# Performance work log

Measured on AMD Instinct MI355X. Metric: run time of the kernel, lower is better.

## Reference

```python
import jax, jax.numpy as jnp
import numpy as np

B, T, C, H = 2, 2048, 1024, 16
HD = C // H  # 64


def setup_inputs() -> dict:
    key = jax.random.key(0)
    ks = jax.random.split(key, 5)
    x = jax.random.normal(ks[0], (B, T, C), jnp.float32)
    scale = 0.02
    Wq = jax.random.normal(ks[1], (C, C), jnp.float32) * scale
    Wk = jax.random.normal(ks[2], (C, C), jnp.float32) * scale
    Wv = jax.random.normal(ks[3], (C, C), jnp.float32) * scale
    Wo = jax.random.normal(ks[4], (C, C), jnp.float32) * scale
    # RoPE tables: freqs_cis = exp(i * pos * theta_j), theta_j = 10000^(-2j/HD)
    pos = jnp.arange(T, dtype=jnp.float32)
    theta = 10000.0 ** (-jnp.arange(0, HD, 2, dtype=jnp.float32) / HD)  # [HD/2]
    ang = pos[:, None] * theta[None, :]  # [T, HD/2]
    cos = jnp.cos(ang)
    sin = jnp.sin(ang)
    return {"x": x, "Wq": Wq, "Wk": Wk, "Wv": Wv, "Wo": Wo, "cos": cos, "sin": sin}


def _rope(t, cos, sin):
    # t: [B,T,H,HD]; pairs (even, odd) along last dim form complex numbers
    b, s, h, hd = t.shape
    tr = t.reshape(b, s, h, hd // 2, 2)
    t0, t1 = tr[..., 0], tr[..., 1]
    c = cos[None, :, None, :]  # [1,T,1,HD/2]
    sn = sin[None, :, None, :]
    o0 = t0 * c - t1 * sn
    o1 = t0 * sn + t1 * c
    return jnp.stack([o0, o1], axis=-1).reshape(b, s, h, hd)


def reference(x, Wq, Wk, Wv, Wo, cos, sin):
    b, t, c = x.shape
    h, hd = H, c // H
    q = (x @ Wq.T).reshape(b, t, h, hd)
    k = (x @ Wk.T).reshape(b, t, h, hd)
    v = (x @ Wv.T).reshape(b, t, h, hd)
    q = _rope(q, cos, sin)
    k = _rope(k, cos, sin)
    # explicit causal attention with full TxT score matrix (as in source)
    att = jnp.einsum("bthd,bshd->bhts", q, k) / jnp.sqrt(jnp.float32(hd))
    causal = jnp.tril(jnp.ones((t, t), dtype=bool))
    att = jnp.where(causal[None, None, :, :], att, -jnp.inf)
    att = jax.nn.softmax(att, axis=-1)
    out = jnp.einsum("bhts,bshd->bthd", att, v).reshape(b, t, c)
    return out @ Wo.T
```

## Files before the change

kernel.cpp:

```cpp
#include <hip/hip_runtime.h>
#include <cstdint>
#include <cstddef>


typedef __bf16 bf16;
typedef float  f32x4  __attribute__((ext_vector_type(4)));
typedef __bf16 bf16x4 __attribute__((ext_vector_type(4)));
typedef __bf16 bf16x8 __attribute__((ext_vector_type(8)));

constexpr int Bb = 2, Tt = 2048, Cc = 1024, Hh = 16;
constexpr int Mrows = Bb * Tt;
constexpr int NT = Tt / 64;
constexpr int LDS_ = 72;

#define GLOAD_LDS16(gp, lp)                                                      \
    __builtin_amdgcn_global_load_lds(                                            \
        (const __attribute__((address_space(1))) void*)(gp),                     \
        (__attribute__((address_space(3))) void*)(lp), 16, 0, 0)

#define QUAD_T(v0, v1, v2, v3, c2)                                               \
    {                                                                            \
        float e0 = (c2 & 1) ? v0 : v1, e1 = (c2 & 1) ? v2 : v3;                  \
        e0 = __shfl_xor(e0, 1); e1 = __shfl_xor(e1, 1);                          \
        if (c2 & 1) { v0 = e0; v2 = e1; } else { v1 = e0; v3 = e1; }             \
        float f0 = (c2 & 2) ? v0 : v2, f1 = (c2 & 2) ? v1 : v3;                  \
        f0 = __shfl_xor(f0, 2); f1 = __shfl_xor(f1, 2);                          \
        if (c2 & 2) { v0 = f0; v1 = f1; } else { v2 = f0; v3 = f1; }             \
    }

__global__ __launch_bounds__(256) void convert_k(const float* __restrict__ x,
                                                 const float* __restrict__ Wq,
                                                 const float* __restrict__ Wk,
                                                 const float* __restrict__ Wv,
                                                 const float* __restrict__ Wo,
                                                 const float* __restrict__ cosb,
                                                 const float* __restrict__ sinb,
                                                 bf16* __restrict__ xb,
                                                 bf16* __restrict__ Wqkv,
                                                 bf16* __restrict__ Wob,
                                                 float2* __restrict__ cs)
{
    if (blockIdx.x >= 4096) {
        int pi = ((blockIdx.x - 4096) * 256 + threadIdx.x) * 8;
#pragma unroll
        for (int u = 0; u < 8; ++u)
            cs[pi + u] = float2{cosb[pi + u], sinb[pi + u]};
        return;
    }
    uint32_t id = blockIdx.x * 256 + threadIdx.x;
    const float* src; bf16* dst; float sc = 1.0f;
    if (id < 524288u) {
        uint32_t tile = id >> 10, slot = id & 1023;
        uint32_t row = (tile >> 4) * 128 + (slot >> 9) * 64 +
                       ((slot >> 6) & 3) * 16 + (slot & 15);
        uint32_t k = (tile & 15) * 64 + ((slot >> 8) & 1) * 32 + ((slot >> 4) & 3) * 8;
        src = x + (size_t)row * 1024 + k;
        dst = xb + (size_t)id * 8;
    } else if (id < 917504u) {
        uint32_t t2 = id - 524288u;
        uint32_t tile = t2 >> 10, slot = t2 & 1023;
        uint32_t n = (tile >> 4) * 128 + (slot >> 9) * 64 +
                     ((slot >> 6) & 3) * 16 + (slot & 15);
        uint32_t k = (tile & 15) * 64 + ((slot >> 8) & 1) * 32 + ((slot >> 4) & 3) * 8;
        if (n < 1024)      { src = Wq + (size_t)n * 1024 + k;
                             sc = 0.125f * 1.44269504088896f; }
        else if (n < 2048)   src = Wk + (size_t)(n - 1024) * 1024 + k;
        else                 src = Wv + (size_t)(n - 2048) * 1024 + k;
        dst = Wqkv + (size_t)t2 * 8;
    } else {
        uint32_t t3 = id - 917504u;
        uint32_t tile = t3 >> 9, slot = t3 & 511;
        uint32_t n = (tile >> 4) * 64 + (slot >> 8) * 32 +
                     ((slot >> 6) & 1) * 16 + (slot & 15);
        uint32_t k = (tile & 15) * 64 + ((slot >> 7) & 1) * 32 + ((slot >> 4) & 3) * 8;
        src = Wo + (size_t)n * 1024 + k;
        dst = Wob + (size_t)t3 * 8;
    }
    float4 v0 = *(const float4*)(src);
    float4 v1 = *(const float4*)(src + 4);
    bf16x8 t;
    t[0] = (bf16)(v0.x*sc); t[1] = (bf16)(v0.y*sc); t[2] = (bf16)(v0.z*sc); t[3] = (bf16)(v0.w*sc);
    t[4] = (bf16)(v1.x*sc); t[5] = (bf16)(v1.y*sc); t[6] = (bf16)(v1.z*sc); t[7] = (bf16)(v1.w*sc);
    *(bf16x8*)dst = t;
}

__global__ __launch_bounds__(256) void gemm_qkv(const bf16* __restrict__ A,
                                                const bf16* __restrict__ W,
                                                bf16* __restrict__ QK,
                                                bf16* __restrict__ Vt,
                                                const float2* __restrict__ cs)
{
    __shared__ bf16 As[8192];
    __shared__ bf16 Ws[8192];
    const int tid  = threadIdx.x;
    const int lane = tid & 63, wave = tid >> 6;
    const int rhw = wave >> 1, chw = wave & 1;
    const int wr = rhw * 64, wc = chw * 64;
    const int l16 = lane & 15, lq = lane >> 4;
    const int row0 = blockIdx.x * 128, col0 = blockIdx.y * 128;

    f32x4 acc[4][4];
#pragma unroll
    for (int i = 0; i < 4; ++i)
#pragma unroll
        for (int j = 0; j < 4; ++j) acc[i][j] = f32x4{0.f, 0.f, 0.f, 0.f};

    const bf16* At = A + (size_t)blockIdx.x * 16 * 8192;
    const bf16* Wt = W + (size_t)blockIdx.y * 16 * 8192;

    for (int kb = 0; kb < 16; ++kb) {
        const bf16* at = At + kb * 8192;
        const bf16* wt = Wt + kb * 8192;
#pragma unroll
        for (int rnd = 0; rnd < 4; ++rnd) {
            const int seg = rnd * 4 + wave;
            GLOAD_LDS16(at + seg * 512 + lane * 8, &As[seg * 512]);
            GLOAD_LDS16(wt + seg * 512 + lane * 8, &Ws[seg * 512]);
        }
        __syncthreads();
#pragma unroll
        for (int ks = 0; ks < 2; ++ks) {
            bf16x8 af[4], bfr[4];
#pragma unroll
            for (int i = 0; i < 4; ++i)
                af[i] = *(const bf16x8*)(&As[(rhw * 512 + ks * 256 + i * 64 + lq * 16 + l16) * 8]);
#pragma unroll
            for (int j = 0; j < 4; ++j)
                bfr[j] = *(const bf16x8*)(&Ws[(chw * 512 + ks * 256 + j * 64 + lq * 16 + l16) * 8]);
#pragma unroll
            for (int i = 0; i < 4; ++i)
#pragma unroll
                for (int j = 0; j < 4; ++j)
                    acc[i][j] = __builtin_amdgcn_mfma_f32_16x16x32_bf16(
                        af[i], bfr[j], acc[i][j], 0, 0, 0);
        }
        __syncthreads();
    }

    const int c2 = l16 & 3, g4 = (l16 >> 2) * 4;
    if (blockIdx.y < 16) {
#pragma unroll
        for (int i = 0; i < 4; ++i)
#pragma unroll
            for (int j = 0; j < 4; ++j) {
                float v0 = acc[i][j][0], v1 = acc[i][j][1];
                float v2 = acc[i][j][2], v3 = acc[i][j][3];
                QUAD_T(v0, v1, v2, v3, c2);
                const int row = row0 + wr + i * 16 + lq * 4 + c2;
                const int t   = row & (Tt - 1);
                const int colb = wc + j * 16 + g4;
                const int p0   = (colb & 63) >> 1;
                float4 cp = *(const float4*)(&cs[t * 32 + p0]);
                bf16x4 pk;
                pk[0] = (bf16)(v0 * cp.x - v1 * cp.y);
                pk[1] = (bf16)(v0 * cp.y + v1 * cp.x);
                pk[2] = (bf16)(v2 * cp.z - v3 * cp.w);
                pk[3] = (bf16)(v2 * cp.w + v3 * cp.z);
                *(bf16x4*)(&QK[(size_t)row * 2048 + col0 + colb]) = pk;
            }
    } else {
#pragma unroll
        for (int i = 0; i < 4; ++i)
#pragma unroll
            for (int j = 0; j < 4; ++j) {
                const int dfull = col0 - 2048 + wc + j * 16 + l16;
                const int h = dfull >> 6, d = dfull & 63;
                const int row = row0 + wr + i * 16 + lq * 4;
                const int b = row >> 11, t = row & (Tt - 1);
                bf16x4 pk;
                pk[0] = (bf16)acc[i][j][0]; pk[1] = (bf16)acc[i][j][1];
                pk[2] = (bf16)acc[i][j][2]; pk[3] = (bf16)acc[i][j][3];
                *(bf16x4*)(&Vt[((size_t)(b * 16 + h) * 64 + d) * (size_t)Tt + t]) = pk;
            }
    }
}

__global__ __launch_bounds__(256) void gemm_o(const bf16* __restrict__ A,
                                              const bf16* __restrict__ W,
                                              float* __restrict__ Out)
{
    __shared__ bf16 As[8192];
    __shared__ bf16 Ws[4096];
    const int tid  = threadIdx.x;
    const int lane = tid & 63, wave = tid >> 6;
    const int rhw = wave >> 1, chw = wave & 1;
    const int wr = rhw * 64, wc = chw * 32;
    const int l16 = lane & 15, lq = lane >> 4;
    const int row0 = blockIdx.x * 128, col0 = blockIdx.y * 64;

    f32x4 acc[4][2];
#pragma unroll
    for (int i = 0; i < 4; ++i)
#pragma unroll
        for (int j = 0; j < 2; ++j) acc[i][j] = f32x4{0.f, 0.f, 0.f, 0.f};

    const bf16* At = A + (size_t)blockIdx.x * 16 * 8192;
    const bf16* Wt = W + (size_t)blockIdx.y * 16 * 4096;

    for (int kb = 0; kb < 16; ++kb) {
        const bf16* at = At + kb * 8192;
        const bf16* wt = Wt + kb * 4096;
#pragma unroll
        for (int rnd = 0; rnd < 4; ++rnd) {
            const int seg = rnd * 4 + wave;
            GLOAD_LDS16(at + seg * 512 + lane * 8, &As[seg * 512]);
        }
#pragma unroll
        for (int rnd = 0; rnd < 2; ++rnd) {
            const int seg = rnd * 4 + wave;
            GLOAD_LDS16(wt + seg * 512 + lane * 8, &Ws[seg * 512]);
        }
        __syncthreads();
#pragma unroll
        for (int ks = 0; ks < 2; ++ks) {
            bf16x8 af[4], bfr[2];
#pragma unroll
            for (int i = 0; i < 4; ++i)
                af[i] = *(const bf16x8*)(&As[(rhw * 512 + ks * 256 + i * 64 + lq * 16 + l16) * 8]);
#pragma unroll
            for (int j = 0; j < 2; ++j)
                bfr[j] = *(const bf16x8*)(&Ws[(chw * 256 + ks * 128 + j * 64 + lq * 16 + l16) * 8]);
#pragma unroll
            for (int i = 0; i < 4; ++i)
#pragma unroll
                for (int j = 0; j < 2; ++j)
                    acc[i][j] = __builtin_amdgcn_mfma_f32_16x16x32_bf16(
                        af[i], bfr[j], acc[i][j], 0, 0, 0);
        }
        __syncthreads();
    }
    const int c2 = l16 & 3, g4 = (l16 >> 2) * 4;
#pragma unroll
    for (int i = 0; i < 4; ++i)
#pragma unroll
        for (int j = 0; j < 2; ++j) {
            float v0 = acc[i][j][0], v1 = acc[i][j][1];
            float v2 = acc[i][j][2], v3 = acc[i][j][3];
            QUAD_T(v0, v1, v2, v3, c2);
            const int row = row0 + wr + i * 16 + lq * 4 + c2;
            const int col = col0 + wc + j * 16 + g4;
            *(float4*)(&Out[(size_t)row * Cc + col]) = float4{v0, v1, v2, v3};
        }
}

__global__ __launch_bounds__(256, 4) void attn_k(const bf16* __restrict__ QK,
                                                 const bf16* __restrict__ Vt,
                                                 bf16* __restrict__ O)
{
    __shared__ bf16 Ks[2][64 * LDS_];
    __shared__ bf16 Vs[2][64 * LDS_];
    const int tid = threadIdx.x;
    const int wv = tid >> 6, lane = tid & 63;
    const int l16 = lane & 15, lq = lane >> 4;
    const int id = blockIdx.y * 16 + blockIdx.x;
    const int bh = (id & 7) * 4 + (id >> 7);
    const int pi = (id >> 3) & 15;
    const int b = bh >> 4, h = bh & 15;
    const int kr = tid >> 2, c0 = (tid & 3) * 16;
    const int pr = 32 * (kr >> 5) + 16 * ((kr >> 2) & 1) + 4 * ((kr >> 3) & 3) + (kr & 3);

    const bf16* kcol = QK + 1024 + (size_t)(b * Tt + kr) * 2048 + h * 64 + c0;
    const bf16* vcol = Vt + ((size_t)bh * 64 + kr) * Tt + c0;

    for (int phase = 0; phase < 2; ++phase) {
        const int qt = phase ? pi : (NT - 1 - pi);

        const int qglob = qt * 64 + wv * 16 + l16;
        const bf16* qp = QK + (size_t)(b * Tt + qglob) * 2048 + h * 64;
        bf16x8 qf0 = *(const bf16x8*)(qp + lq * 8);
        bf16x8 qf1 = *(const bf16x8*)(qp + 32 + lq * 8);

        uint4 pk0 = *(const uint4*)(kcol);
        uint4 pk1 = *(const uint4*)(kcol + 8);
        uint4 pv0 = *(const uint4*)(vcol);
        uint4 pv1 = *(const uint4*)(vcol + 8);
        *(uint4*)(&Ks[0][pr * LDS_ + c0])     = pk0;
        *(uint4*)(&Ks[0][pr * LDS_ + c0 + 8]) = pk1;
        *(uint4*)(&Vs[0][kr * LDS_ + c0])     = pv0;
        *(uint4*)(&Vs[0][kr * LDS_ + c0 + 8]) = pv1;
        __syncthreads();

        float l = 0.f;
        f32x4 o[4];
#pragma unroll
        for (int dt = 0; dt < 4; ++dt) o[dt] = f32x4{0.f, 0.f, 0.f, 0.f};

        for (int t = 0; t <= qt; ++t) {
            const int cur = t & 1;
            if (t < qt) {
                const bf16* kn = kcol + (size_t)(t + 1) * 64 * 2048;
                const bf16* vn = vcol + (t + 1) * 64;
                pk0 = *(const uint4*)(kn);
                pk1 = *(const uint4*)(kn + 8);
                pv0 = *(const uint4*)(vn);
                pv1 = *(const uint4*)(vn + 8);
            }

            f32x4 s[4];
#pragma unroll
            for (int mt = 0; mt < 4; ++mt) s[mt] = f32x4{0.f, 0.f, 0.f, 0.f};
#pragma unroll
            for (int mt = 0; mt < 4; ++mt) {
                bf16x8 a0 = *(const bf16x8*)(&Ks[cur][(mt * 16 + l16) * LDS_ + lq * 8]);
                s[mt] = __builtin_amdgcn_mfma_f32_16x16x32_bf16(a0, qf0, s[mt], 0, 0, 0);
            }
#pragma unroll
            for (int mt = 0; mt < 4; ++mt) {
                bf16x8 a1 = *(const bf16x8*)(&Ks[cur][(mt * 16 + l16) * LDS_ + 32 + lq * 8]);
                s[mt] = __builtin_amdgcn_mfma_f32_16x16x32_bf16(a1, qf1, s[mt], 0, 0, 0);
            }
            if (t == qt) {
                const int qloc = wv * 16 + l16;
#pragma unroll
                for (int mt = 0; mt < 4; ++mt)
#pragma unroll
                    for (int r = 0; r < 4; ++r) {
                        int keyl = (mt >> 1) * 32 + lq * 8 + (mt & 1) * 4 + r;
                        if (keyl > qloc) s[mt][r] = -1e30f;
                    }
            }
            bf16x8 pb0, pb1;
#pragma unroll
            for (int mt = 0; mt < 4; ++mt)
#pragma unroll
                for (int r = 0; r < 4; ++r) {
                    float p = exp2f(s[mt][r]);
                    l += p;
                    s[mt][r] = p;
                }
#pragma unroll
            for (int r = 0; r < 4; ++r) {
                pb0[r]     = (bf16)s[0][r];
                pb0[4 + r] = (bf16)s[1][r];
                pb1[r]     = (bf16)s[2][r];
                pb1[4 + r] = (bf16)s[3][r];
            }
#pragma unroll
            for (int dt = 0; dt < 4; ++dt) {
                bf16x8 v0 = *(const bf16x8*)(&Vs[cur][(dt * 16 + l16) * LDS_ + lq * 8]);
                o[dt] = __builtin_amdgcn_mfma_f32_16x16x32_bf16(v0, pb0, o[dt], 0, 0, 0);
            }
#pragma unroll
            for (int dt = 0; dt < 4; ++dt) {
                bf16x8 v1 = *(const bf16x8*)(&Vs[cur][(dt * 16 + l16) * LDS_ + 32 + lq * 8]);
                o[dt] = __builtin_amdgcn_mfma_f32_16x16x32_bf16(v1, pb1, o[dt], 0, 0, 0);
            }
            if (t < qt) {
                *(uint4*)(&Ks[cur ^ 1][pr * LDS_ + c0])     = pk0;
                *(uint4*)(&Ks[cur ^ 1][pr * LDS_ + c0 + 8]) = pk1;
                *(uint4*)(&Vs[cur ^ 1][kr * LDS_ + c0])     = pv0;
                *(uint4*)(&Vs[cur ^ 1][kr * LDS_ + c0 + 8]) = pv1;
            }
            __syncthreads();
        }
        l += __shfl_xor(l, 16);
        l += __shfl_xor(l, 32);
        float inv = 1.f / l;
        bf16* obase = O + ((size_t)(b * 16 + (qt >> 1)) * 16 + h) * 8192;
        const int rh = qt & 1;
#pragma unroll
        for (int dt = 0; dt < 4; ++dt) {
            bf16x4 pk;
#pragma unroll
            for (int r = 0; r < 4; ++r) pk[r] = (bf16)(o[dt][r] * inv);
            const int slot = rh * 512 + (dt >> 1) * 256 + wv * 64 +
                             ((dt & 1) * 2 + (lq >> 1)) * 16 + l16;
            *(bf16x4*)(obase + slot * 8 + (lq & 1) * 4) = pk;
        }
    }
}

extern "C" void kernel_launch(void* const* d_in, const int* in_sizes, int n_in,
                              void* d_out, int out_size, void* d_ws, size_t ws_size,
                              hipStream_t stream)
{
    const float* x    = (const float*)d_in[0];
    const float* Wq   = (const float*)d_in[1];
    const float* Wk   = (const float*)d_in[2];
    const float* Wv   = (const float*)d_in[3];
    const float* Wo   = (const float*)d_in[4];
    const float* cosb = (const float*)d_in[5];
    const float* sinb = (const float*)d_in[6];

    constexpr size_t M1 = 1024 * 1024;
    bf16* base = (bf16*)d_ws;
    bf16*   xb   = base;
    bf16*   QK   = base + 4 * M1;
    bf16*   VtG  = base + 12 * M1;
    bf16*   Wqkv = base + 16 * M1;
    bf16*   Wob  = base + 19 * M1;
    float2* csT  = (float2*)(base + 20 * M1);
    bf16*   Ow   = xb;

    convert_k<<<4096 + 32, 256, 0, stream>>>(x, Wq, Wk, Wv, Wo, cosb, sinb,
                                             xb, Wqkv, Wob, csT);

    gemm_qkv<<<dim3(Mrows / 128, 3072 / 128), 256, 0, stream>>>(
        xb, Wqkv, QK, VtG, csT);

    attn_k<<<dim3(NT / 2, Bb * Hh), 256, 0, stream>>>(QK, VtG, Ow);

    gemm_o<<<dim3(Mrows / 128, Cc / 64), 256, 0, stream>>>(Ow, Wob, (float*)d_out);
}
```

Measured before the change: 175.5 us.

## Launch one attention block per query tile and compute row sums via MFMA

The attention kernel no longer pairs a long and a short query tile in one block. It launches one block per query tile (1024 blocks instead of 512) with a remapped id that orders tiles from heavy to light in rounds, to improve load balance and occupancy. The softmax denominator is now accumulated with an extra MFMA against a ones vector instead of scalar adds followed by cross-lane shuffles. The trade-off is two extra MFMAs per iteration and more blocks that each reload their own K/V tiles.

Result: faster. 169.2 us (-3.6%).

```diff
diff --git a/kernel.cpp b/kernel.cpp
--- a/kernel.cpp
+++ b/kernel.cpp
@@ -252,9 +252,11 @@
     const int tid = threadIdx.x;
     const int wv = tid >> 6, lane = tid & 63;
     const int l16 = lane & 15, lq = lane >> 4;
-    const int id = blockIdx.y * 16 + blockIdx.x;
-    const int bh = (id & 7) * 4 + (id >> 7);
-    const int pi = (id >> 3) & 15;
+    const int id = blockIdx.y * gridDim.x + blockIdx.x;
+    const int bh = (id & 7) * 4 + ((id >> 3) & 3);
+    const int sIdx = (id >> 5) & 7, rnd4 = id >> 8;
+    const int qt = (rnd4 == 0) ? 31 - sIdx : (rnd4 == 1) ? 16 + sIdx
+                 : (rnd4 == 2) ? 15 - sIdx : sIdx;
     const int b = bh >> 4, h = bh & 15;
     const int kr = tid >> 2, c0 = (tid & 3) * 16;
     const int pr = 32 * (kr >> 5) + 16 * ((kr >> 2) & 1) + 4 * ((kr >> 3) & 3) + (kr & 3);
@@ -262,111 +264,108 @@
     const bf16* kcol = QK + 1024 + (size_t)(b * Tt + kr) * 2048 + h * 64 + c0;
     const bf16* vcol = Vt + ((size_t)bh * 64 + kr) * Tt + c0;
 
-    for (int phase = 0; phase < 2; ++phase) {
-        const int qt = phase ? pi : (NT - 1 - pi);
-
-        const int qglob = qt * 64 + wv * 16 + l16;
-        const bf16* qp = QK + (size_t)(b * Tt + qglob) * 2048 + h * 64;
-        bf16x8 qf0 = *(const bf16x8*)(qp + lq * 8);
-        bf16x8 qf1 = *(const bf16x8*)(qp + 32 + lq * 8);
-
-        uint4 pk0 = *(const uint4*)(kcol);
-        uint4 pk1 = *(const uint4*)(kcol + 8);
-        uint4 pv0 = *(const uint4*)(vcol);
-        uint4 pv1 = *(const uint4*)(vcol + 8);
-        *(uint4*)(&Ks[0][pr * LDS_ + c0])     = pk0;
-        *(uint4*)(&Ks[0][pr * LDS_ + c0 + 8]) = pk1;
-        *(uint4*)(&Vs[0][kr * LDS_ + c0])     = pv0;
-        *(uint4*)(&Vs[0][kr * LDS_ + c0 + 8]) = pv1;
+    const int qglob = qt * 64 + wv * 16 + l16;
+    const bf16* qp = QK + (size_t)(b * Tt + qglob) * 2048 + h * 64;
+    bf16x8 qf0 = *(const bf16x8*)(qp + lq * 8);
+    bf16x8 qf1 = *(const bf16x8*)(qp + 32 + lq * 8);
+
+    bf16x8 onef;
+#pragma unroll
+    for (int r = 0; r < 8; ++r) onef[r] = (bf16)1.0f;
+
+    uint4 pk0 = *(const uint4*)(kcol);
+    uint4 pk1 = *(const uint4*)(kcol + 8);
+    uint4 pv0 = *(const uint4*)(vcol);
+    uint4 pv1 = *(const uint4*)(vcol + 8);
+    *(uint4*)(&Ks[0][pr * LDS_ + c0])     = pk0;
+    *(uint4*)(&Ks[0][pr * LDS_ + c0 + 8]) = pk1;
+    *(uint4*)(&Vs[0][kr * LDS_ + c0])     = pv0;
+    *(uint4*)(&Vs[0][kr * LDS_ + c0 + 8]) = pv1;
+    __syncthreads();
+
+    f32x4 accl = f32x4{0.f, 0.f, 0.f, 0.f};
+    f32x4 o[4];
+#pragma unroll
+    for (int dt = 0; dt < 4; ++dt) o[dt] = f32x4{0.f, 0.f, 0.f, 0.f};
+
+    for (int t = 0; t <= qt; ++t) {
+        const int cur = t & 1;
+        if (t < qt) {
+            const bf16* kn = kcol + (size_t)(t + 1) * 64 * 2048;
+            const bf16* vn = vcol + (t + 1) * 64;
+            pk0 = *(const uint4*)(kn);
+            pk1 = *(const uint4*)(kn + 8);
+            pv0 = *(const uint4*)(vn);
+            pv1 = *(const uint4*)(vn + 8);
+        }
+
+        f32x4 s[4];
+#pragma unroll
+        for (int mt = 0; mt < 4; ++mt) s[mt] = f32x4{0.f, 0.f, 0.f, 0.f};
+#pragma unroll
+        for (int mt = 0; mt < 4; ++mt) {
+            bf16x8 a0 = *(const bf16x8*)(&Ks[cur][(mt * 16 + l16) * LDS_ + lq * 8]);
+            s[mt] = __builtin_amdgcn_mfma_f32_16x16x32_bf16(a0, qf0, s[mt], 0, 0, 0);
+        }
+#pragma unroll
+        for (int mt = 0; mt < 4; ++mt) {
+            bf16x8 a1 = *(const bf16x8*)(&Ks[cur][(mt * 16 + l16) * LDS_ + 32 + lq * 8]);
+            s[mt] = __builtin_amdgcn_mfma_f32_16x16x32_bf16(a1, qf1, s[mt], 0, 0, 0);
+        }
+        if (t == qt) {
+            const int qloc = wv * 16 + l16;
+#pragma unroll
+            for (int mt = 0; mt < 4; ++mt)
+#pragma unroll
+                for (int r = 0; r < 4; ++r) {
+                    int keyl = (mt >> 1) * 32 + lq * 8 + (mt & 1) * 4 + r;
+                    if (keyl > qloc) s[mt][r] = -1e30f;
+                }
+        }
+        bf16x8 pb0, pb1;
+#pragma unroll
+        for (int mt = 0; mt < 4; ++mt)
+#pragma unroll
+            for (int r = 0; r < 4; ++r)
+                s[mt][r] = exp2f(s[mt][r]);
+#pragma unroll
+        for (int r = 0; r < 4; ++r) {
+            pb0[r]     = (bf16)s[0][r];
+            pb0[4 + r] = (bf16)s[1][r];
+            pb1[r]     = (bf16)s[2][r];
+            pb1[4 + r] = (bf16)s[3][r];
+        }
+        accl = __builtin_amdgcn_mfma_f32_16x16x32_bf16(onef, pb0, accl, 0, 0, 0);
+        accl = __builtin_amdgcn_mfma_f32_16x16x32_bf16(onef, pb1, accl, 0, 0, 0);
+#pragma unroll
+        for (int dt = 0; dt < 4; ++dt) {
+            bf16x8 v0 = *(const bf16x8*)(&Vs[cur][(dt * 16 + l16) * LDS_ + lq * 8]);
+            o[dt] = __builtin_amdgcn_mfma_f32_16x16x32_bf16(v0, pb0, o[dt], 0, 0, 0);
+        }
+#pragma unroll
+        for (int dt = 0; dt < 4; ++dt) {
+            bf16x8 v1 = *(const bf16x8*)(&Vs[cur][(dt * 16 + l16) * LDS_ + 32 + lq * 8]);
+            o[dt] = __builtin_amdgcn_mfma_f32_16x16x32_bf16(v1, pb1, o[dt], 0, 0, 0);
+        }
+        if (t < qt) {
+            *(uint4*)(&Ks[cur ^ 1][pr * LDS_ + c0])     = pk0;
+            *(uint4*)(&Ks[cur ^ 1][pr * LDS_ + c0 + 8]) = pk1;
+            *(uint4*)(&Vs[cur ^ 1][kr * LDS_ + c0])     = pv0;
+            *(uint4*)(&Vs[cur ^ 1][kr * LDS_ + c0 + 8]) = pv1;
+        }
         __syncthreads();
-
-        float l = 0.f;
-        f32x4 o[4];
-#pragma unroll
-        for (int dt = 0; dt < 4; ++dt) o[dt] = f32x4{0.f, 0.f, 0.f, 0.f};
-
-        for (int t = 0; t <= qt; ++t) {
-            const int cur = t & 1;
-            if (t < qt) {
-                const bf16* kn = kcol + (size_t)(t + 1) * 64 * 2048;
-                const bf16* vn = vcol + (t + 1) * 64;
-                pk0 = *(const uint4*)(kn);
-                pk1 = *(const uint4*)(kn + 8);
-                pv0 = *(const uint4*)(vn);
-                pv1 = *(const uint4*)(vn + 8);
-            }
-
-            f32x4 s[4];
-#pragma unroll
-            for (int mt = 0; mt < 4; ++mt) s[mt] = f32x4{0.f, 0.f, 0.f, 0.f};
-#pragma unroll
-            for (int mt = 0; mt < 4; ++mt) {
-                bf16x8 a0 = *(const bf16x8*)(&Ks[cur][(mt * 16 + l16) * LDS_ + lq * 8]);
-                s[mt] = __builtin_amdgcn_mfma_f32_16x16x32_bf16(a0, qf0, s[mt], 0, 0, 0);
-            }
-#pragma unroll
-            for (int mt = 0; mt < 4; ++mt) {
-                bf16x8 a1 = *(const bf16x8*)(&Ks[cur][(mt * 16 + l16) * LDS_ + 32 + lq * 8]);
-                s[mt] = __builtin_amdgcn_mfma_f32_16x16x32_bf16(a1, qf1, s[mt], 0, 0, 0);
-            }
-            if (t == qt) {
-                const int qloc = wv * 16 + l16;
-#pragma unroll
-                for (int mt = 0; mt < 4; ++mt)
-#pragma unroll
-                    for (int r = 0; r < 4; ++r) {
-                        int keyl = (mt >> 1) * 32 + lq * 8 + (mt & 1) * 4 + r;
-                        if (keyl > qloc) s[mt][r] = -1e30f;
-                    }
-            }
-            bf16x8 pb0, pb1;
-#pragma unroll
-            for (int mt = 0; mt < 4; ++mt)
-#pragma unroll
-                for (int r = 0; r < 4; ++r) {
-                    float p = exp2f(s[mt][r]);
-                    l += p;
-                    s[mt][r] = p;
-                }
-#pragma unroll
-            for (int r = 0; r < 4; ++r) {
-                pb0[r]     = (bf16)s[0][r];
-                pb0[4 + r] = (bf16)s[1][r];
-                pb1[r]     = (bf16)s[2][r];
-                pb1[4 + r] = (bf16)s[3][r];
-            }
-#pragma unroll
-            for (int dt = 0; dt < 4; ++dt) {
-                bf16x8 v0 = *(const bf16x8*)(&Vs[cur][(dt * 16 + l16) * LDS_ + lq * 8]);
-                o[dt] = __builtin_amdgcn_mfma_f32_16x16x32_bf16(v0, pb0, o[dt], 0, 0, 0);
-            }
-#pragma unroll
-            for (int dt = 0; dt < 4; ++dt) {
-                bf16x8 v1 = *(const bf16x8*)(&Vs[cur][(dt * 16 + l16) * LDS_ + 32 + lq * 8]);
-                o[dt] = __builtin_amdgcn_mfma_f32_16x16x32_bf16(v1, pb1, o[dt], 0, 0, 0);
-            }
-            if (t < qt) {
-                *(uint4*)(&Ks[cur ^ 1][pr * LDS_ + c0])     = pk0;
-                *(uint4*)(&Ks[cur ^ 1][pr * LDS_ + c0 + 8]) = pk1;
-                *(uint4*)(&Vs[cur ^ 1][kr * LDS_ + c0])     = pv0;
-                *(uint4*)(&Vs[cur ^ 1][kr * LDS_ + c0 + 8]) = pv1;
-            }
-            __syncthreads();
-        }
-        l += __shfl_xor(l, 16);
-        l += __shfl_xor(l, 32);
-        float inv = 1.f / l;
-        bf16* obase = O + ((size_t)(b * 16 + (qt >> 1)) * 16 + h) * 8192;
-        const int rh = qt & 1;
-#pragma unroll
-        for (int dt = 0; dt < 4; ++dt) {
-            bf16x4 pk;
-#pragma unroll
-            for (int r = 0; r < 4; ++r) pk[r] = (bf16)(o[dt][r] * inv);
-            const int slot = rh * 512 + (dt >> 1) * 256 + wv * 64 +
-                             ((dt & 1) * 2 + (lq >> 1)) * 16 + l16;
-            *(bf16x4*)(obase + slot * 8 + (lq & 1) * 4) = pk;
-        }
+    }
+    float inv = 1.f / accl[0];
+    bf16* obase = O + ((size_t)(b * 16 + (qt >> 1)) * 16 + h) * 8192;
+    const int rh = qt & 1;
+#pragma unroll
+    for (int dt = 0; dt < 4; ++dt) {
+        bf16x4 pk;
+#pragma unroll
+        for (int r = 0; r < 4; ++r) pk[r] = (bf16)(o[dt][r] * inv);
+        const int slot = rh * 512 + (dt >> 1) * 256 + wv * 64 +
+                         ((dt & 1) * 2 + (lq >> 1)) * 16 + l16;
+        *(bf16x4*)(obase + slot * 8 + (lq & 1) * 4) = pk;
     }
 }
 
@@ -398,7 +397,7 @@
     gemm_qkv<<<dim3(Mrows / 128, 3072 / 128), 256, 0, stream>>>(
         xb, Wqkv, QK, VtG, csT);
 
-    attn_k<<<dim3(NT / 2, Bb * Hh), 256, 0, stream>>>(QK, VtG, Ow);
+    attn_k<<<dim3(NT, Bb * Hh), 256, 0, stream>>>(QK, VtG, Ow);
 
     gemm_o<<<dim3(Mrows / 128, Cc / 64), 256, 0, stream>>>(Ow, Wob, (float*)d_out);
 }
```
